# Optimization experiments

Measured on AMD Instinct MI355X. Metric: run time of the kernel, lower is better.

Reference implementation:

```python
import jax, jax.numpy as jnp
import numpy as np
from jax import lax

DIM = 256          # C
D_INNER = 512      # expand * dim
D_STATE = 16       # N
DT_RANK = 32       # ceil(d_inner / 16)
K_CONV = 4


def setup_inputs() -> dict:
    key = jax.random.key(0)
    ks = jax.random.split(key, 20)
    B, C, H, W = 2, DIM, 64, 64
    Di, N, R = D_INNER, D_STATE, DT_RANK
    s = 0.02
    inp = {
        "decoder_feat": jax.random.normal(ks[0], (B, C, H, W), jnp.float32),
        "encoder_feat": jax.random.normal(ks[1], (B, C, H, W), jnp.float32),
        # CrossMambaFusion params
        "dec_w": jax.random.normal(ks[2], (C, 2 * Di), jnp.float32) * s,
        "dec_b": jnp.zeros((2 * Di,), jnp.float32),
        "enc_w": jax.random.normal(ks[3], (C, Di), jnp.float32) * s,
        "enc_b": jnp.zeros((Di,), jnp.float32),
        "out_w": jax.random.normal(ks[4], (Di, C), jnp.float32) * s,
        "out_b": jnp.zeros((C,), jnp.float32),
        "ln_g": jnp.ones((C,), jnp.float32),
        "ln_b": jnp.zeros((C,), jnp.float32),
        # Mamba block params (inner dim = Di, expand=1.0)
        "in_w": jax.random.normal(ks[5], (Di, 2 * Di), jnp.float32) * s,
        "in_b": jnp.zeros((2 * Di,), jnp.float32),
        "conv_w": jax.random.normal(ks[6], (Di, 1, K_CONV), jnp.float32) * 0.1,
        "conv_b": jnp.zeros((Di,), jnp.float32),
        "x_proj_w": jax.random.normal(ks[7], (Di, R + 2 * N), jnp.float32) * s,
        "dt_w": jax.random.normal(ks[8], (R, Di), jnp.float32) * 0.1,
        "dt_b": jax.random.uniform(ks[9], (Di,), jnp.float32, -4.0, -2.0),  # small dt after softplus
        "A_log": jnp.log(jnp.tile(jnp.arange(1, N + 1, dtype=jnp.float32)[None, :], (Di, 1))),
        "D_param": jnp.ones((Di,), jnp.float32),
        "m_out_w": jax.random.normal(ks[10], (Di, Di), jnp.float32) * s,
        "m_out_b": jnp.zeros((Di,), jnp.float32),
    }
    return inp


def _mamba(x, in_w, in_b, conv_w, conv_b, x_proj_w, dt_w, dt_b, A_log, D_param, m_out_w, m_out_b):
    # x: (B, L, Di)
    Bsz, L, Di = x.shape
    N, R = D_STATE, DT_RANK
    xz = x @ in_w + in_b                      # (B, L, 2*Di)
    xm, z = jnp.split(xz, 2, axis=-1)
    # causal depthwise conv over the sequence axis
    xc = jnp.swapaxes(xm, 1, 2)               # (B, Di, L)
    xc = lax.conv_general_dilated(
        xc, conv_w, window_strides=(1,), padding=[(K_CONV - 1, 0)],
        dimension_numbers=("NCH", "OIH", "NCH"), feature_group_count=Di)
    xc = xc + conv_b[None, :, None]
    u = jax.nn.silu(jnp.swapaxes(xc, 1, 2))   # (B, L, Di)
    x_dbl = u @ x_proj_w                      # (B, L, R+2N)
    dt = jax.nn.softplus(x_dbl[..., :R] @ dt_w + dt_b)   # (B, L, Di)
    Bm = x_dbl[..., R:R + N]                  # (B, L, N)
    Cm = x_dbl[..., R + N:]                   # (B, L, N)
    A = -jnp.exp(A_log)                       # (Di, N)

    def step(h, t):
        dt_t, u_t, B_t, C_t = t               # (B,Di),(B,Di),(B,N),(B,N)
        dA = jnp.exp(dt_t[..., None] * A)     # (B, Di, N)
        h = h * dA + (dt_t * u_t)[..., None] * B_t[:, None, :]
        y = jnp.einsum("bdn,bn->bd", h, C_t)
        return h, y

    h0 = jnp.zeros((Bsz, Di, N), x.dtype)
    _, ys = lax.scan(step, h0, (jnp.swapaxes(dt, 0, 1), jnp.swapaxes(u, 0, 1),
                                jnp.swapaxes(Bm, 0, 1), jnp.swapaxes(Cm, 0, 1)))
    y = jnp.swapaxes(ys, 0, 1) + u * D_param  # skip connection via D
    y = y * jax.nn.silu(z)
    return y @ m_out_w + m_out_b


def reference(decoder_feat, encoder_feat, dec_w, dec_b, enc_w, enc_b, out_w, out_b,
              ln_g, ln_b, in_w, in_b, conv_w, conv_b, x_proj_w, dt_w, dt_b,
              A_log, D_param, m_out_w, m_out_b):
    B, C, H, W = decoder_feat.shape
    Di = D_INNER
    dec = jnp.transpose(decoder_feat, (0, 2, 3, 1)).reshape(B, H * W, C)
    enc = jnp.transpose(encoder_feat, (0, 2, 3, 1)).reshape(B, H * W, C)
    dec_proj = dec @ dec_w + dec_b
    dec_x, dec_gate = dec_proj[..., :Di], dec_proj[..., Di:]
    enc_p = enc @ enc_w + enc_b
    combined = dec_x * jax.nn.sigmoid(enc_p) + enc_p          # (B, L, Di)
    processed = _mamba(combined, in_w, in_b, conv_w, conv_b, x_proj_w,
                       dt_w, dt_b, A_log, D_param, m_out_w, m_out_b)
    out = (processed * jax.nn.sigmoid(dec_gate)) @ out_w + out_b
    res = out + dec
    mu = jnp.mean(res, axis=-1, keepdims=True)
    var = jnp.mean(jnp.square(res - mu), axis=-1, keepdims=True)
    res = (res - mu) * lax.rsqrt(var + 1e-5) * ln_g + ln_b
    return jnp.transpose(res.reshape(B, H, W, C), (0, 3, 1, 2))
```

## Files before the change

kernel.cpp:

```cpp
#include <hip/hip_runtime.h>
#include <hip/hip_bf16.h>

typedef __bf16 bf16x8_t __attribute__((ext_vector_type(8)));
typedef float f32x4_t __attribute__((ext_vector_type(4)));

__device__ __forceinline__ float sigmoidf_(float x) { return 1.0f / (1.0f + __expf(-x)); }
__device__ __forceinline__ float siluf_(float x) { return x * sigmoidf_(x); }
__device__ __forceinline__ float softplusf_(float x) {
    return fmaxf(x, 0.0f) + log1pf(__expf(-fabsf(x)));
}
__device__ __forceinline__ float b2f(ushort u) { return __uint_as_float(((unsigned)u) << 16); }

__global__ __launch_bounds__(256) void k_cast_w(
    const float* __restrict__ dec_w, const float* __restrict__ enc_w,
    const float* __restrict__ in_w, const float* __restrict__ m_out_w,
    const float* __restrict__ out_w, const float* __restrict__ x_proj_w,
    const float* __restrict__ dt_w,
    __hip_bfloat16* __restrict__ dec_wT, __hip_bfloat16* __restrict__ enc_wT,
    __hip_bfloat16* __restrict__ in_wT, __hip_bfloat16* __restrict__ m_out_wT,
    __hip_bfloat16* __restrict__ out_wT, __hip_bfloat16* __restrict__ xpwT,
    __hip_bfloat16* __restrict__ dtwT)
{
    int gid = blockIdx.x * 256 + threadIdx.x;
    const float* src; __hip_bfloat16* dst; int lk, N, idx;
    if (gid < 262144)       { src = dec_w;    dst = dec_wT;   lk = 8; N = 1024; idx = gid; }
    else if (gid < 393216)  { src = enc_w;    dst = enc_wT;   lk = 8; N = 512;  idx = gid - 262144; }
    else if (gid < 917504)  { src = in_w;     dst = in_wT;    lk = 9; N = 1024; idx = gid - 393216; }
    else if (gid < 1179648) { src = m_out_w;  dst = m_out_wT; lk = 9; N = 512;  idx = gid - 917504; }
    else if (gid < 1310720) { src = out_w;    dst = out_wT;   lk = 9; N = 256;  idx = gid - 1179648; }
    else if (gid < 1343488) { src = x_proj_w; dst = xpwT;     lk = 9; N = 64;   idx = gid - 1310720; }
    else                    { src = dt_w;     dst = dtwT;     lk = 5; N = 512;  idx = gid - 1343488; }
    int K = 1 << lk;
    int n = idx >> lk, k = idx & (K - 1);
    dst[idx] = __float2bfloat16(src[(size_t)k * N + n]);
}

__global__ __launch_bounds__(256) void k_tr_in(
    const float* __restrict__ dec, const float* __restrict__ enc,
    __hip_bfloat16* __restrict__ decL, __hip_bfloat16* __restrict__ encL)
{
    __shared__ float tile[64][65];
    const int t = threadIdx.x;
    const int ct = blockIdx.x & 3;
    const int lt = (blockIdx.x >> 2) & 63;
    const int sel = blockIdx.x >> 8;
    const int b = sel & 1, ten = sel >> 1;
    const float* src = ten ? enc : dec;
    __hip_bfloat16* dst = ten ? encL : decL;
    const size_t ibase = (size_t)b * 256 * 4096 + (size_t)(ct * 64) * 4096 + (size_t)lt * 64;
#pragma unroll
    for (int i = 0; i < 16; ++i) {
        int c = i * 4 + (t >> 6), l = t & 63;
        tile[c][l] = src[ibase + (size_t)c * 4096 + l];
    }
    __syncthreads();
    const size_t obase = ((size_t)b * 4096 + (size_t)lt * 64) * 256 + ct * 64;
#pragma unroll
    for (int i = 0; i < 16; ++i) {
        int l = i * 4 + (t >> 6), c = t & 63;
        dst[obase + (size_t)l * 256 + c] = __float2bfloat16(tile[c][l]);
    }
}

template <int EPI, int K>
__global__ __launch_bounds__(256) void bgemm(
    const __hip_bfloat16* __restrict__ A, const __hip_bfloat16* __restrict__ Bt,
    const float* __restrict__ bias, void* __restrict__ out0,
    void* __restrict__ out1, const void* __restrict__ extra)
{
    __shared__ ushort At[128 * 32];
    __shared__ ushort Bl[128 * 32];
    const int tid = threadIdx.x;
    const int wave = tid >> 6, lane = tid & 63;
    const int n0 = blockIdx.x * 128, m0 = blockIdx.y * 128;
    const int wm = (wave >> 1) * 64, wn = (wave & 1) * 64;
    f32x4_t acc[4][4] = {};
    const int fr = lane & 15, fq = (lane >> 4) * 8;

    for (int k0 = 0; k0 < K; k0 += 32) {
#pragma unroll
        for (int q = 0; q < 2; ++q) {
            int idx = q * 256 + tid;
            int row = idx >> 2, ch = (idx & 3) * 8;
            uint4 va = *(const uint4*)&A[(size_t)(m0 + row) * K + k0 + ch];
            uint4 vb = *(const uint4*)&Bt[(size_t)(n0 + row) * K + k0 + ch];
            *(uint4*)&At[row * 32 + ch] = va;
            *(uint4*)&Bl[row * 32 + ch] = vb;
        }
        __syncthreads();
        bf16x8_t af[4], bf[4];
#pragma unroll
        for (int i = 0; i < 4; ++i) {
            af[i] = *(bf16x8_t*)&At[(wm + i * 16 + fr) * 32 + fq];
            bf[i] = *(bf16x8_t*)&Bl[(wn + i * 16 + fr) * 32 + fq];
        }
#pragma unroll
        for (int i = 0; i < 4; ++i)
#pragma unroll
            for (int j = 0; j < 4; ++j)
                acc[i][j] = __builtin_amdgcn_mfma_f32_16x16x32_bf16(af[i], bf[j], acc[i][j], 0, 0, 0);
        __syncthreads();
    }

    const int col = lane & 15, rbase = (lane >> 4) * 4;
#pragma unroll
    for (int i = 0; i < 4; ++i) {
#pragma unroll
        for (int j = 0; j < 4; ++j) {
#pragma unroll
            for (int r = 0; r < 4; ++r) {
                int m = m0 + wm + i * 16 + rbase + r;
                int n = n0 + wn + j * 16 + col;
                float v = acc[i][j][r] + bias[n];
                if (EPI == 0) {
                    ((__hip_bfloat16*)out0)[(size_t)m * 512 + n] = __float2bfloat16(v);
                } else if (EPI == 1) {
                    if (n < 512) {
                        float ep = __bfloat162float(((const __hip_bfloat16*)extra)[(size_t)m * 512 + n]);
                        ((__hip_bfloat16*)out0)[(size_t)m * 512 + n] =
                            __float2bfloat16(fmaf(v, sigmoidf_(ep), ep));
                    } else {
                        ((__hip_bfloat16*)out1)[(size_t)m * 512 + (n - 512)] =
                            __float2bfloat16(sigmoidf_(v));
                    }
                } else if (EPI == 2) {
                    if (n < 512)
                        ((__hip_bfloat16*)out0)[(size_t)m * 512 + n] = __float2bfloat16(v);
                    else
                        ((__hip_bfloat16*)out1)[(size_t)m * 512 + (n - 512)] =
                            __float2bfloat16(siluf_(v));
                } else if (EPI == 3) {
                    float g = __bfloat162float(((const __hip_bfloat16*)extra)[(size_t)m * 512 + n]);
                    ((__hip_bfloat16*)out0)[(size_t)m * 512 + n] = __float2bfloat16(v * g);
                } else {
                    float dv = __bfloat162float(((const __hip_bfloat16*)extra)[(size_t)m * 256 + n]);
                    ((float*)out0)[(size_t)m * 256 + n] = v + dv;
                }
            }
        }
    }
}

#define CROWS 16
__global__ __launch_bounds__(256) void k_conv_proj(
    const __hip_bfloat16* __restrict__ xm, const float* __restrict__ conv_w,
    const float* __restrict__ conv_b, const __hip_bfloat16* __restrict__ xpwT,
    const __hip_bfloat16* __restrict__ dtwT, const float* __restrict__ dt_b,
    __hip_bfloat16* __restrict__ u_out, float* __restrict__ Bm,
    float* __restrict__ Cm, float* __restrict__ dt_out)
{
    __shared__ ushort ut[CROWS][512 + 8];
    __shared__ ushort adt[CROWS][32 + 8];
    const int tid = threadIdx.x;
    const int wave = tid >> 6, lane = tid & 63;
    const int bl0 = blockIdx.x * CROWS;
    const int l0 = bl0 & 4095;
    const int fr = lane & 15, fq = (lane >> 4) * 8;
    const int col = lane & 15, rbase = (lane >> 4) * 4;

    {
        const int d0 = tid * 2;
        float cw0[4], cw1[4];
#pragma unroll
        for (int k = 0; k < 4; ++k) {
            cw0[k] = conv_w[d0 * 4 + k];
            cw1[k] = conv_w[d0 * 4 + 4 + k];
        }
        const float cb0 = conv_b[d0], cb1 = conv_b[d0 + 1];
        float xa[CROWS + 3], xb[CROWS + 3];
        const ushort* xs = (const ushort*)xm;
#pragma unroll
        for (int i = 0; i < CROWS + 3; ++i) {
            if (l0 - 3 + i >= 0) {
                ushort2 v = *(const ushort2*)&xs[(size_t)(bl0 - 3 + i) * 512 + d0];
                xa[i] = b2f(v.x); xb[i] = b2f(v.y);
            } else { xa[i] = 0.f; xb[i] = 0.f; }
        }
#pragma unroll
        for (int r = 0; r < CROWS; ++r) {
            float a = cb0, b = cb1;
#pragma unroll
            for (int k = 0; k < 4; ++k) {
                a = fmaf(cw0[k], xa[r + k], a);
                b = fmaf(cw1[k], xb[r + k], b);
            }
            float ua = siluf_(a), ub = siluf_(b);
            ushort2 up = make_ushort2(
                (ushort)(__bfloat16_as_ushort(__float2bfloat16(ua))),
                (ushort)(__bfloat16_as_ushort(__float2bfloat16(ub))));
            *(ushort2*)&ut[r][d0] = up;
            *(ushort2*)&((ushort*)u_out)[(size_t)(bl0 + r) * 512 + d0] = up;
        }
    }
    __syncthreads();

    {
        f32x4_t acc = {};
        const __hip_bfloat16* bp = xpwT + (size_t)(wave * 16 + fr) * 512;
#pragma unroll
        for (int k0 = 0; k0 < 512; k0 += 32) {
            bf16x8_t af = *(bf16x8_t*)&ut[fr][k0 + fq];
            bf16x8_t bf = *(const bf16x8_t*)&bp[k0 + fq];
            acc = __builtin_amdgcn_mfma_f32_16x16x32_bf16(af, bf, acc, 0, 0, 0);
        }
#pragma unroll
        for (int r = 0; r < 4; ++r) {
            int m = rbase + r;
            int n = wave * 16 + col;
            float v = acc[r];
            if (n < 32)      adt[m][n] = (ushort)__bfloat16_as_ushort(__float2bfloat16(v));
            else if (n < 48) Bm[(size_t)(bl0 + m) * 16 + (n - 32)] = v;
            else             Cm[(size_t)(bl0 + m) * 16 + (n - 48)] = v;
        }
    }
    __syncthreads();

    {
        bf16x8_t af = *(bf16x8_t*)&adt[fr][fq];
#pragma unroll
        for (int t = 0; t < 8; ++t) {
            int nt = wave * 8 + t;
            bf16x8_t bf = *(const bf16x8_t*)&dtwT[(size_t)(nt * 16 + fr) * 32 + fq];
            f32x4_t acc = {};
            acc = __builtin_amdgcn_mfma_f32_16x16x32_bf16(af, bf, acc, 0, 0, 0);
#pragma unroll
            for (int r = 0; r < 4; ++r) {
                int m = rbase + r;
                int n = nt * 16 + col;
                dt_out[(size_t)(bl0 + m) * 512 + n] = softplusf_(acc[r] + dt_b[n]);
            }
        }
    }
}

#define CHUNK 32
#define NCHUNK 128

__global__ __launch_bounds__(512) void k_scan_part(
    const float* __restrict__ dt, const __hip_bfloat16* __restrict__ u,
    const float* __restrict__ Bmp, const float* __restrict__ A_log,
    float* __restrict__ hpart, float* __restrict__ decay)
{
    __shared__ float Bs[CHUNK * 16];
    const int d = threadIdx.x;
    const int chunk = blockIdx.x & (NCHUNK - 1);
    const int b = blockIdx.x >> 7;
    const size_t row0 = (size_t)b * 4096 + (size_t)chunk * CHUNK;

    Bs[d] = Bmp[row0 * 16 + d];
    float Av[16];
#pragma unroll
    for (int n = 0; n < 16; n += 4) {
        float4 al = *(const float4*)&A_log[d * 16 + n];
        Av[n + 0] = -__expf(al.x);
        Av[n + 1] = -__expf(al.y);
        Av[n + 2] = -__expf(al.z);
        Av[n + 3] = -__expf(al.w);
    }
    __syncthreads();

    const float* dtp = dt + row0 * 512 + d;
    const __hip_bfloat16* up = u + row0 * 512 + d;
    float h[16] = {};
    float dtsum = 0.f;
    for (int t = 0; t < CHUNK; ++t) {
        float dtv = dtp[(size_t)t * 512];
        float uv = __bfloat162float(up[(size_t)t * 512]);
        float dtu = dtv * uv;
        dtsum += dtv;
        const float* Bt = &Bs[t * 16];
#pragma unroll
        for (int n = 0; n < 16; ++n)
            h[n] = fmaf(h[n], __expf(dtv * Av[n]), dtu * Bt[n]);
    }
    const size_t idx = (((size_t)b * NCHUNK + chunk) * 512 + d) * 16;
#pragma unroll
    for (int n = 0; n < 16; n += 4)
        *(float4*)&hpart[idx + n] = make_float4(h[n], h[n + 1], h[n + 2], h[n + 3]);
#pragma unroll
    for (int n = 0; n < 16; n += 4)
        *(float4*)&decay[idx + n] = make_float4(
            __expf(Av[n] * dtsum), __expf(Av[n + 1] * dtsum),
            __expf(Av[n + 2] * dtsum), __expf(Av[n + 3] * dtsum));
}

__global__ __launch_bounds__(256) void k_scan_comb(
    const float* __restrict__ hpart, const float* __restrict__ decay,
    float* __restrict__ h_in)
{
    const int gid = blockIdx.x * 256 + threadIdx.x;
    const int n = gid & 15;
    const int d = (gid >> 4) & 511;
    const int b = gid >> 13;
    float h = 0.f;
    for (int c = 0; c < NCHUNK; ++c) {
        const size_t idx = (((size_t)b * NCHUNK + c) * 512 + d) * 16 + n;
        h_in[idx] = h;
        h = fmaf(h, decay[idx], hpart[idx]);
    }
}

__global__ __launch_bounds__(512) void k_scan_fin(
    const float* __restrict__ dt, const __hip_bfloat16* __restrict__ u,
    const float* __restrict__ Bmp, const float* __restrict__ Cmp,
    const float* __restrict__ A_log, const float* __restrict__ Dp,
    const __hip_bfloat16* __restrict__ zs, const float* __restrict__ h_in,
    __hip_bfloat16* __restrict__ yout)
{
    __shared__ float Bs[CHUNK * 16];
    __shared__ float Cs[CHUNK * 16];
    const int d = threadIdx.x;
    const int chunk = blockIdx.x & (NCHUNK - 1);
    const int b = blockIdx.x >> 7;
    const size_t row0 = (size_t)b * 4096 + (size_t)chunk * CHUNK;

    Bs[d] = Bmp[row0 * 16 + d];
    Cs[d] = Cmp[row0 * 16 + d];
    float Av[16];
#pragma unroll
    for (int n = 0; n < 16; n += 4) {
        float4 al = *(const float4*)&A_log[d * 16 + n];
        Av[n + 0] = -__expf(al.x);
        Av[n + 1] = -__expf(al.y);
        Av[n + 2] = -__expf(al.z);
        Av[n + 3] = -__expf(al.w);
    }
    const float Dv = Dp[d];
    float h[16];
    const size_t idx = (((size_t)b * NCHUNK + chunk) * 512 + d) * 16;
#pragma unroll
    for (int n = 0; n < 16; n += 4) {
        float4 hv = *(const float4*)&h_in[idx + n];
        h[n] = hv.x; h[n + 1] = hv.y; h[n + 2] = hv.z; h[n + 3] = hv.w;
    }
    __syncthreads();

    const float* dtp = dt + row0 * 512 + d;
    const __hip_bfloat16* up = u + row0 * 512 + d;
    const __hip_bfloat16* zp = zs + row0 * 512 + d;
    __hip_bfloat16* yp = yout + row0 * 512 + d;
    for (int t = 0; t < CHUNK; ++t) {
        float dtv = dtp[(size_t)t * 512];
        float uv = __bfloat162float(up[(size_t)t * 512]);
        float zv = __bfloat162float(zp[(size_t)t * 512]);
        float dtu = dtv * uv;
        const float* Bt = &Bs[t * 16];
        const float* Ct = &Cs[t * 16];
        float y = 0.f;
#pragma unroll
        for (int n = 0; n < 16; ++n) {
            h[n] = fmaf(h[n], __expf(dtv * Av[n]), dtu * Bt[n]);
            y = fmaf(h[n], Ct[n], y);
        }
        yp[(size_t)t * 512] = __float2bfloat16((y + uv * Dv) * zv);
    }
}

__global__ __launch_bounds__(256) void k_ln_t(
    const float* __restrict__ res, const float* __restrict__ ln_g,
    const float* __restrict__ ln_b, float* __restrict__ outp)
{
    __shared__ float r[64 * 257];
    __shared__ float red[64][8];
    __shared__ float mu_s[64], sc_s[64];
    const int tid = threadIdx.x;
    const int b = blockIdx.x >> 6;
    const int l0 = (blockIdx.x & 63) * 64;
    const size_t base = ((size_t)b * 4096 + l0) * 256;

    for (int e = tid; e < 64 * 256; e += 256) {
        int i = e >> 8;
        int c = e & 255;
        r[i * 257 + c] = res[base + (size_t)i * 256 + c];
    }
    __syncthreads();
    {
        int i = tid >> 2, s = tid & 3;
        float ps = 0.f, pq = 0.f;
        for (int c = s * 64; c < s * 64 + 64; ++c) {
            float v = r[i * 257 + c];
            ps += v;
            pq = fmaf(v, v, pq);
        }
        red[i][s] = ps;
        red[i][4 + s] = pq;
    }
    __syncthreads();
    if (tid < 64) {
        float ps = red[tid][0] + red[tid][1] + red[tid][2] + red[tid][3];
        float pq = red[tid][4] + red[tid][5] + red[tid][6] + red[tid][7];
        float mu = ps * (1.0f / 256.0f);
        float var = pq * (1.0f / 256.0f) - mu * mu;
        mu_s[tid] = mu;
        sc_s[tid] = rsqrtf(var + 1e-5f);
    }
    __syncthreads();
    const int il = tid & 63;
    const int cg = tid >> 6;
    const float mu = mu_s[il], sc = sc_s[il];
    for (int c = cg; c < 256; c += 4) {
        float v = (r[il * 257 + c] - mu) * sc * ln_g[c] + ln_b[c];
        outp[(size_t)b * (256 * 4096) + (size_t)c * 4096 + l0 + il] = v;
    }
}

extern "C" void kernel_launch(void* const* d_in, const int* in_sizes, int n_in,
                              void* d_out, int out_size, void* d_ws, size_t ws_size,
                              hipStream_t stream)
{
    const float* decoder_feat = (const float*)d_in[0];
    const float* encoder_feat = (const float*)d_in[1];
    const float* dec_w = (const float*)d_in[2];
    const float* dec_b = (const float*)d_in[3];
    const float* enc_w = (const float*)d_in[4];
    const float* enc_b = (const float*)d_in[5];
    const float* out_w = (const float*)d_in[6];
    const float* out_b = (const float*)d_in[7];
    const float* ln_g = (const float*)d_in[8];
    const float* ln_bb = (const float*)d_in[9];
    const float* in_w = (const float*)d_in[10];
    const float* in_b = (const float*)d_in[11];
    const float* conv_w = (const float*)d_in[12];
    const float* conv_b = (const float*)d_in[13];
    const float* x_proj_w = (const float*)d_in[14];
    const float* dt_w = (const float*)d_in[15];
    const float* dt_b = (const float*)d_in[16];
    const float* A_log = (const float*)d_in[17];
    const float* D_param = (const float*)d_in[18];
    const float* m_out_w = (const float*)d_in[19];
    const float* m_out_b = (const float*)d_in[20];

    float* outp = (float*)d_out;
    char* ws = (char*)d_ws;
    const size_t MB = 1024ull * 1024;
    __hip_bfloat16* decL     = (__hip_bfloat16*)(ws + 0 * MB);
    __hip_bfloat16* encL     = (__hip_bfloat16*)(ws + 4 * MB);
    __hip_bfloat16* dec_wT   = (__hip_bfloat16*)(ws + 8 * MB);
    __hip_bfloat16* enc_wT   = (__hip_bfloat16*)(ws + 9 * MB);
    __hip_bfloat16* in_wT    = (__hip_bfloat16*)(ws + 10 * MB);
    __hip_bfloat16* m_out_wT = (__hip_bfloat16*)(ws + 11 * MB);
    __hip_bfloat16* out_wT   = (__hip_bfloat16*)(ws + 12 * MB);
    __hip_bfloat16* xpwT     = (__hip_bfloat16*)(ws + 12 * MB + 262144);
    __hip_bfloat16* dtwT     = (__hip_bfloat16*)(ws + 12 * MB + 262144 + 65536);
    __hip_bfloat16* enc_pb   = (__hip_bfloat16*)(ws + 13 * MB);
    __hip_bfloat16* combined = (__hip_bfloat16*)(ws + 29 * MB);
    __hip_bfloat16* gate_sig = (__hip_bfloat16*)(ws + 37 * MB);
    __hip_bfloat16* xm = (__hip_bfloat16*)(ws + 53 * MB);
    __hip_bfloat16* z_silu = (__hip_bfloat16*)(ws + 61 * MB);
    __hip_bfloat16* u_buf = (__hip_bfloat16*)(ws + 69 * MB);
    float* dt_buf = (float*)(ws + 77 * MB);
    float* Bm = (float*)(ws + 93 * MB);
    float* Cm = (float*)(ws + 93 * MB + 524288);
    float* hpart = (float*)(ws + 13 * MB);
    float* decay = hpart + 2097152;
    float* h_in  = (float*)xm;
    __hip_bfloat16* y_buf = combined;
    __hip_bfloat16* gated = xm;
    float* res = dt_buf;

    k_cast_w<<<5312, 256, 0, stream>>>(dec_w, enc_w, in_w, m_out_w, out_w, x_proj_w, dt_w,
                                       dec_wT, enc_wT, in_wT, m_out_wT, out_wT, xpwT, dtwT);
    k_tr_in<<<1024, 256, 0, stream>>>(decoder_feat, encoder_feat, decL, encL);
    bgemm<0, 256><<<dim3(4, 64), 256, 0, stream>>>(
        encL, enc_wT, enc_b, enc_pb, nullptr, nullptr);
    bgemm<1, 256><<<dim3(8, 64), 256, 0, stream>>>(
        decL, dec_wT, dec_b, combined, gate_sig, enc_pb);
    bgemm<2, 512><<<dim3(8, 64), 256, 0, stream>>>(
        combined, in_wT, in_b, xm, z_silu, nullptr);
    k_conv_proj<<<512, 256, 0, stream>>>(
        xm, conv_w, conv_b, xpwT, dtwT, dt_b, u_buf, Bm, Cm, dt_buf);
    k_scan_part<<<2 * NCHUNK, 512, 0, stream>>>(dt_buf, u_buf, Bm, A_log, hpart, decay);
    k_scan_comb<<<64, 256, 0, stream>>>(hpart, decay, h_in);
    k_scan_fin<<<2 * NCHUNK, 512, 0, stream>>>(
        dt_buf, u_buf, Bm, Cm, A_log, D_param, z_silu, h_in, y_buf);
    bgemm<3, 512><<<dim3(4, 64), 256, 0, stream>>>(
        y_buf, m_out_wT, m_out_b, gated, nullptr, gate_sig);
    bgemm<4, 512><<<dim3(2, 64), 256, 0, stream>>>(
        gated, out_wT, out_b, res, nullptr, decL);
    k_ln_t<<<128, 256, 0, stream>>>(res, ln_g, ln_bb, outp);
}
```

Measured before the change: 297.1 us.

## Fuse prep kernels, dec/enc projections, and output GEMM with LayerNorm

Merges the weight-cast and input-transpose kernels into one launch. It computes the encoder and decoder projections in a single dual-accumulator GEMM, so enc_p never goes through memory. It also fuses the final output GEMM with the residual add and LayerNorm, so the fp32 residual buffer is no longer written and read back. This saves launches and global traffic, but the fused output kernel runs only 64 blocks of 512 threads with large shared memory, which lowers parallelism on a GPU with many CUs.

```diff
diff --git a/kernel.cpp b/kernel.cpp
--- a/kernel.cpp
+++ b/kernel.cpp
@@ -11,39 +11,39 @@
 }
 __device__ __forceinline__ float b2f(ushort u) { return __uint_as_float(((unsigned)u) << 16); }
 
-__global__ __launch_bounds__(256) void k_cast_w(
+__global__ __launch_bounds__(256) void k_prep(
     const float* __restrict__ dec_w, const float* __restrict__ enc_w,
     const float* __restrict__ in_w, const float* __restrict__ m_out_w,
     const float* __restrict__ out_w, const float* __restrict__ x_proj_w,
     const float* __restrict__ dt_w,
+    const float* __restrict__ dec, const float* __restrict__ enc,
     __hip_bfloat16* __restrict__ dec_wT, __hip_bfloat16* __restrict__ enc_wT,
     __hip_bfloat16* __restrict__ in_wT, __hip_bfloat16* __restrict__ m_out_wT,
     __hip_bfloat16* __restrict__ out_wT, __hip_bfloat16* __restrict__ xpwT,
-    __hip_bfloat16* __restrict__ dtwT)
-{
-    int gid = blockIdx.x * 256 + threadIdx.x;
-    const float* src; __hip_bfloat16* dst; int lk, N, idx;
-    if (gid < 262144)       { src = dec_w;    dst = dec_wT;   lk = 8; N = 1024; idx = gid; }
-    else if (gid < 393216)  { src = enc_w;    dst = enc_wT;   lk = 8; N = 512;  idx = gid - 262144; }
-    else if (gid < 917504)  { src = in_w;     dst = in_wT;    lk = 9; N = 1024; idx = gid - 393216; }
-    else if (gid < 1179648) { src = m_out_w;  dst = m_out_wT; lk = 9; N = 512;  idx = gid - 917504; }
-    else if (gid < 1310720) { src = out_w;    dst = out_wT;   lk = 9; N = 256;  idx = gid - 1179648; }
-    else if (gid < 1343488) { src = x_proj_w; dst = xpwT;     lk = 9; N = 64;   idx = gid - 1310720; }
-    else                    { src = dt_w;     dst = dtwT;     lk = 5; N = 512;  idx = gid - 1343488; }
-    int K = 1 << lk;
-    int n = idx >> lk, k = idx & (K - 1);
-    dst[idx] = __float2bfloat16(src[(size_t)k * N + n]);
-}
-
-__global__ __launch_bounds__(256) void k_tr_in(
-    const float* __restrict__ dec, const float* __restrict__ enc,
+    __hip_bfloat16* __restrict__ dtwT,
     __hip_bfloat16* __restrict__ decL, __hip_bfloat16* __restrict__ encL)
 {
     __shared__ float tile[64][65];
+    if (blockIdx.x < 5312) {
+        int gid = blockIdx.x * 256 + threadIdx.x;
+        const float* src; __hip_bfloat16* dst; int lk, N, idx;
+        if (gid < 262144)       { src = dec_w;    dst = dec_wT;   lk = 8; N = 1024; idx = gid; }
+        else if (gid < 393216)  { src = enc_w;    dst = enc_wT;   lk = 8; N = 512;  idx = gid - 262144; }
+        else if (gid < 917504)  { src = in_w;     dst = in_wT;    lk = 9; N = 1024; idx = gid - 393216; }
+        else if (gid < 1179648) { src = m_out_w;  dst = m_out_wT; lk = 9; N = 512;  idx = gid - 917504; }
+        else if (gid < 1310720) { src = out_w;    dst = out_wT;   lk = 9; N = 256;  idx = gid - 1179648; }
+        else if (gid < 1343488) { src = x_proj_w; dst = xpwT;     lk = 9; N = 64;   idx = gid - 1310720; }
+        else                    { src = dt_w;     dst = dtwT;     lk = 5; N = 512;  idx = gid - 1343488; }
+        int K = 1 << lk;
+        int n = idx >> lk, k = idx & (K - 1);
+        dst[idx] = __float2bfloat16(src[(size_t)k * N + n]);
+        return;
+    }
+    const int bid = blockIdx.x - 5312;
     const int t = threadIdx.x;
-    const int ct = blockIdx.x & 3;
-    const int lt = (blockIdx.x >> 2) & 63;
-    const int sel = blockIdx.x >> 8;
+    const int ct = bid & 3;
+    const int lt = (bid >> 2) & 63;
+    const int sel = bid >> 8;
     const int b = sel & 1, ten = sel >> 1;
     const float* src = ten ? enc : dec;
     __hip_bfloat16* dst = ten ? encL : decL;
@@ -59,6 +59,82 @@
     for (int i = 0; i < 16; ++i) {
         int l = i * 4 + (t >> 6), c = t & 63;
         dst[obase + (size_t)l * 256 + c] = __float2bfloat16(tile[c][l]);
+    }
+}
+
+__global__ __launch_bounds__(256) void k_fuse_in(
+    const __hip_bfloat16* __restrict__ decL, const __hip_bfloat16* __restrict__ encL,
+    const __hip_bfloat16* __restrict__ dec_wT, const __hip_bfloat16* __restrict__ enc_wT,
+    const float* __restrict__ dec_b, const float* __restrict__ enc_b,
+    __hip_bfloat16* __restrict__ combined, __hip_bfloat16* __restrict__ gate_sig)
+{
+    __shared__ ushort Ad[128 * 32], Bd[128 * 32], Ae[128 * 32], Be[128 * 32];
+    const int tid = threadIdx.x;
+    const int wave = tid >> 6, lane = tid & 63;
+    const int n0 = blockIdx.x * 128, m0 = blockIdx.y * 128;
+    const bool dual = (n0 < 512);
+    const int wm = (wave >> 1) * 64, wn = (wave & 1) * 64;
+    f32x4_t accd[4][4] = {}, acce[4][4] = {};
+    const int fr = lane & 15, fq = (lane >> 4) * 8;
+
+    for (int k0 = 0; k0 < 256; k0 += 32) {
+#pragma unroll
+        for (int q = 0; q < 2; ++q) {
+            int idx = q * 256 + tid;
+            int row = idx >> 2, ch = (idx & 3) * 8;
+            *(uint4*)&Ad[row * 32 + ch] = *(const uint4*)&decL[(size_t)(m0 + row) * 256 + k0 + ch];
+            *(uint4*)&Bd[row * 32 + ch] = *(const uint4*)&dec_wT[(size_t)(n0 + row) * 256 + k0 + ch];
+            if (dual) {
+                *(uint4*)&Ae[row * 32 + ch] = *(const uint4*)&encL[(size_t)(m0 + row) * 256 + k0 + ch];
+                *(uint4*)&Be[row * 32 + ch] = *(const uint4*)&enc_wT[(size_t)(n0 + row) * 256 + k0 + ch];
+            }
+        }
+        __syncthreads();
+        bf16x8_t ad[4], bd[4];
+#pragma unroll
+        for (int i = 0; i < 4; ++i) {
+            ad[i] = *(bf16x8_t*)&Ad[(wm + i * 16 + fr) * 32 + fq];
+            bd[i] = *(bf16x8_t*)&Bd[(wn + i * 16 + fr) * 32 + fq];
+        }
+#pragma unroll
+        for (int i = 0; i < 4; ++i)
+#pragma unroll
+            for (int j = 0; j < 4; ++j)
+                accd[i][j] = __builtin_amdgcn_mfma_f32_16x16x32_bf16(ad[i], bd[j], accd[i][j], 0, 0, 0);
+        if (dual) {
+            bf16x8_t ae[4], be[4];
+#pragma unroll
+            for (int i = 0; i < 4; ++i) {
+                ae[i] = *(bf16x8_t*)&Ae[(wm + i * 16 + fr) * 32 + fq];
+                be[i] = *(bf16x8_t*)&Be[(wn + i * 16 + fr) * 32 + fq];
+            }
+#pragma unroll
+            for (int i = 0; i < 4; ++i)
+#pragma unroll
+                for (int j = 0; j < 4; ++j)
+                    acce[i][j] = __builtin_amdgcn_mfma_f32_16x16x32_bf16(ae[i], be[j], acce[i][j], 0, 0, 0);
+        }
+        __syncthreads();
+    }
+
+    const int col = lane & 15, rbase = (lane >> 4) * 4;
+#pragma unroll
+    for (int i = 0; i < 4; ++i) {
+#pragma unroll
+        for (int j = 0; j < 4; ++j) {
+#pragma unroll
+            for (int r = 0; r < 4; ++r) {
+                int m = m0 + wm + i * 16 + rbase + r;
+                int n = n0 + wn + j * 16 + col;
+                float vd = accd[i][j][r] + dec_b[n];
+                if (dual) {
+                    float ve = acce[i][j][r] + enc_b[n];
+                    combined[(size_t)m * 512 + n] = __float2bfloat16(fmaf(vd, sigmoidf_(ve), ve));
+                } else {
+                    gate_sig[(size_t)m * 512 + (n - 512)] = __float2bfloat16(sigmoidf_(vd));
+                }
+            }
+        }
     }
 }
 
@@ -112,29 +188,15 @@
                 int m = m0 + wm + i * 16 + rbase + r;
                 int n = n0 + wn + j * 16 + col;
                 float v = acc[i][j][r] + bias[n];
-                if (EPI == 0) {
-                    ((__hip_bfloat16*)out0)[(size_t)m * 512 + n] = __float2bfloat16(v);
-                } else if (EPI == 1) {
-                    if (n < 512) {
-                        float ep = __bfloat162float(((const __hip_bfloat16*)extra)[(size_t)m * 512 + n]);
-                        ((__hip_bfloat16*)out0)[(size_t)m * 512 + n] =
-                            __float2bfloat16(fmaf(v, sigmoidf_(ep), ep));
-                    } else {
-                        ((__hip_bfloat16*)out1)[(size_t)m * 512 + (n - 512)] =
-                            __float2bfloat16(sigmoidf_(v));
-                    }
-                } else if (EPI == 2) {
+                if (EPI == 2) {
                     if (n < 512)
                         ((__hip_bfloat16*)out0)[(size_t)m * 512 + n] = __float2bfloat16(v);
                     else
                         ((__hip_bfloat16*)out1)[(size_t)m * 512 + (n - 512)] =
                             __float2bfloat16(siluf_(v));
-                } else if (EPI == 3) {
+                } else {
                     float g = __bfloat162float(((const __hip_bfloat16*)extra)[(size_t)m * 512 + n]);
                     ((__hip_bfloat16*)out0)[(size_t)m * 512 + n] = __float2bfloat16(v * g);
-                } else {
-                    float dv = __bfloat162float(((const __hip_bfloat16*)extra)[(size_t)m * 256 + n]);
-                    ((float*)out0)[(size_t)m * 256 + n] = v + dv;
                 }
             }
         }
@@ -356,51 +418,107 @@
     }
 }
 
-__global__ __launch_bounds__(256) void k_ln_t(
-    const float* __restrict__ res, const float* __restrict__ ln_g,
-    const float* __restrict__ ln_b, float* __restrict__ outp)
-{
-    __shared__ float r[64 * 257];
-    __shared__ float red[64][8];
-    __shared__ float mu_s[64], sc_s[64];
+__global__ __launch_bounds__(512) void k_out_ln(
+    const __hip_bfloat16* __restrict__ A, const __hip_bfloat16* __restrict__ Bt,
+    const float* __restrict__ bias, const __hip_bfloat16* __restrict__ decL,
+    const float* __restrict__ ln_g, const float* __restrict__ ln_b,
+    float* __restrict__ outp)
+{
+    __shared__ __align__(16) char sm[70912];
+    ushort* At = (ushort*)sm;
+    ushort* Bl = (ushort*)(sm + 8192);
+    float (*lr)[257] = (float(*)[257])sm;
+    float* lred = (float*)(sm + 65792);
+    float* lmu  = (float*)(sm + 69888);
+    float* lsc  = (float*)(sm + 70144);
+
     const int tid = threadIdx.x;
-    const int b = blockIdx.x >> 6;
-    const int l0 = (blockIdx.x & 63) * 64;
-    const size_t base = ((size_t)b * 4096 + l0) * 256;
-
-    for (int e = tid; e < 64 * 256; e += 256) {
-        int i = e >> 8;
-        int c = e & 255;
-        r[i * 257 + c] = res[base + (size_t)i * 256 + c];
-    }
-    __syncthreads();
-    {
-        int i = tid >> 2, s = tid & 3;
-        float ps = 0.f, pq = 0.f;
-        for (int c = s * 64; c < s * 64 + 64; ++c) {
-            float v = r[i * 257 + c];
-            ps += v;
-            pq = fmaf(v, v, pq);
-        }
-        red[i][s] = ps;
-        red[i][4 + s] = pq;
-    }
-    __syncthreads();
-    if (tid < 64) {
-        float ps = red[tid][0] + red[tid][1] + red[tid][2] + red[tid][3];
-        float pq = red[tid][4] + red[tid][5] + red[tid][6] + red[tid][7];
-        float mu = ps * (1.0f / 256.0f);
-        float var = pq * (1.0f / 256.0f) - mu * mu;
-        mu_s[tid] = mu;
-        sc_s[tid] = rsqrtf(var + 1e-5f);
-    }
-    __syncthreads();
-    const int il = tid & 63;
-    const int cg = tid >> 6;
-    const float mu = mu_s[il], sc = sc_s[il];
-    for (int c = cg; c < 256; c += 4) {
-        float v = (r[il * 257 + c] - mu) * sc * ln_g[c] + ln_b[c];
-        outp[(size_t)b * (256 * 4096) + (size_t)c * 4096 + l0 + il] = v;
+    const int wave = tid >> 6, lane = tid & 63;
+    const int m0 = blockIdx.x * 128;
+    const int wm = (wave >> 2) * 64, wn = (wave & 3) * 64;
+    f32x4_t acc[4][4] = {};
+    const int fr = lane & 15, fq = (lane >> 4) * 8;
+
+    for (int k0 = 0; k0 < 512; k0 += 32) {
+        {
+            int row = tid >> 2, ch = (tid & 3) * 8;
+            *(uint4*)&At[row * 32 + ch] = *(const uint4*)&A[(size_t)(m0 + row) * 512 + k0 + ch];
+        }
+#pragma unroll
+        for (int q = 0; q < 2; ++q) {
+            int idx = q * 512 + tid;
+            int row = idx >> 2, ch = (idx & 3) * 8;
+            *(uint4*)&Bl[row * 32 + ch] = *(const uint4*)&Bt[(size_t)row * 512 + k0 + ch];
+        }
+        __syncthreads();
+        bf16x8_t af[4], bf[4];
+#pragma unroll
+        for (int i = 0; i < 4; ++i) {
+            af[i] = *(bf16x8_t*)&At[(wm + i * 16 + fr) * 32 + fq];
+            bf[i] = *(bf16x8_t*)&Bl[(wn + i * 16 + fr) * 32 + fq];
+        }
+#pragma unroll
+        for (int i = 0; i < 4; ++i)
+#pragma unroll
+            for (int j = 0; j < 4; ++j)
+                acc[i][j] = __builtin_amdgcn_mfma_f32_16x16x32_bf16(af[i], bf[j], acc[i][j], 0, 0, 0);
+        __syncthreads();
+    }
+
+    const int col = lane & 15, rbase = (lane >> 4) * 4;
+    for (int mh = 0; mh < 2; ++mh) {
+        if ((wm >> 6) == mh) {
+#pragma unroll
+            for (int i = 0; i < 4; ++i)
+#pragma unroll
+                for (int j = 0; j < 4; ++j)
+#pragma unroll
+                    for (int r = 0; r < 4; ++r) {
+                        int rl = i * 16 + rbase + r;
+                        int n = wn + j * 16 + col;
+                        int m = m0 + mh * 64 + rl;
+                        float dv = b2f(((const ushort*)decL)[(size_t)m * 256 + n]);
+                        lr[rl][n] = acc[i][j][r] + bias[n] + dv;
+                    }
+        }
+        __syncthreads();
+        {
+            int i = tid >> 3, s = tid & 7;
+            float ps = 0.f, pq = 0.f;
+#pragma unroll 8
+            for (int k = 0; k < 32; ++k) {
+                float v = lr[i][s + 8 * k];
+                ps += v;
+                pq = fmaf(v, v, pq);
+            }
+            lred[i * 16 + s] = ps;
+            lred[i * 16 + 8 + s] = pq;
+        }
+        __syncthreads();
+        if (tid < 64) {
+            float ps = 0.f, pq = 0.f;
+#pragma unroll
+            for (int s = 0; s < 8; ++s) {
+                ps += lred[tid * 16 + s];
+                pq += lred[tid * 16 + 8 + s];
+            }
+            float mu = ps * (1.0f / 256.0f);
+            float var = pq * (1.0f / 256.0f) - mu * mu;
+            lmu[tid] = mu;
+            lsc[tid] = rsqrtf(var + 1e-5f);
+        }
+        __syncthreads();
+        {
+            int l = tid & 63;
+            int m = m0 + mh * 64 + l;
+            int bb = m >> 12, lpos = m & 4095;
+            float mu = lmu[l], sc = lsc[l];
+            for (int c = tid >> 6; c < 256; c += 8) {
+                float v = (lr[l][c] - mu) * sc * ln_g[c] + ln_b[c];
+                outp[(size_t)bb * (256 * 4096) + (size_t)c * 4096 + lpos] = v;
+            }
+        }
+        __syncthreads();
     }
 }
 
@@ -442,29 +560,26 @@
     __hip_bfloat16* out_wT   = (__hip_bfloat16*)(ws + 12 * MB);
     __hip_bfloat16* xpwT     = (__hip_bfloat16*)(ws + 12 * MB + 262144);
     __hip_bfloat16* dtwT     = (__hip_bfloat16*)(ws + 12 * MB + 262144 + 65536);
-    __hip_bfloat16* enc_pb   = (__hip_bfloat16*)(ws + 13 * MB);
+    float* hpart             = (float*)(ws + 13 * MB);
+    float* decay             = hpart + 2097152;
     __hip_bfloat16* combined = (__hip_bfloat16*)(ws + 29 * MB);
     __hip_bfloat16* gate_sig = (__hip_bfloat16*)(ws + 37 * MB);
-    __hip_bfloat16* xm = (__hip_bfloat16*)(ws + 53 * MB);
-    __hip_bfloat16* z_silu = (__hip_bfloat16*)(ws + 61 * MB);
-    __hip_bfloat16* u_buf = (__hip_bfloat16*)(ws + 69 * MB);
-    float* dt_buf = (float*)(ws + 77 * MB);
-    float* Bm = (float*)(ws + 93 * MB);
-    float* Cm = (float*)(ws + 93 * MB + 524288);
-    float* hpart = (float*)(ws + 13 * MB);
-    float* decay = hpart + 2097152;
-    float* h_in  = (float*)xm;
-    __hip_bfloat16* y_buf = combined;
-    __hip_bfloat16* gated = xm;
-    float* res = dt_buf;
-
-    k_cast_w<<<5312, 256, 0, stream>>>(dec_w, enc_w, in_w, m_out_w, out_w, x_proj_w, dt_w,
-                                       dec_wT, enc_wT, in_wT, m_out_wT, out_wT, xpwT, dtwT);
-    k_tr_in<<<1024, 256, 0, stream>>>(decoder_feat, encoder_feat, decL, encL);
-    bgemm<0, 256><<<dim3(4, 64), 256, 0, stream>>>(
-        encL, enc_wT, enc_b, enc_pb, nullptr, nullptr);
-    bgemm<1, 256><<<dim3(8, 64), 256, 0, stream>>>(
-        decL, dec_wT, dec_b, combined, gate_sig, enc_pb);
+    __hip_bfloat16* xm       = (__hip_bfloat16*)(ws + 53 * MB);
+    __hip_bfloat16* z_silu   = (__hip_bfloat16*)(ws + 61 * MB);
+    __hip_bfloat16* u_buf    = (__hip_bfloat16*)(ws + 69 * MB);
+    float* dt_buf            = (float*)(ws + 77 * MB);
+    float* Bm                = (float*)(ws + 93 * MB);
+    float* Cm                = (float*)(ws + 93 * MB + 524288);
+    float* h_in              = (float*)xm;
+    __hip_bfloat16* y_buf    = combined;
+    __hip_bfloat16* gated    = xm;
+
+    k_prep<<<6336, 256, 0, stream>>>(
+        dec_w, enc_w, in_w, m_out_w, out_w, x_proj_w, dt_w,
+        decoder_feat, encoder_feat,
+        dec_wT, enc_wT, in_wT, m_out_wT, out_wT, xpwT, dtwT, decL, encL);
+    k_fuse_in<<<dim3(8, 64), 256, 0, stream>>>(
+        decL, encL, dec_wT, enc_wT, dec_b, enc_b, combined, gate_sig);
     bgemm<2, 512><<<dim3(8, 64), 256, 0, stream>>>(
         combined, in_wT, in_b, xm, z_silu, nullptr);
     k_conv_proj<<<512, 256, 0, stream>>>(
@@ -475,7 +590,6 @@
         dt_buf, u_buf, Bm, Cm, A_log, D_param, z_silu, h_in, y_buf);
     bgemm<3, 512><<<dim3(4, 64), 256, 0, stream>>>(
         y_buf, m_out_wT, m_out_b, gated, nullptr, gate_sig);
-    bgemm<4, 512><<<dim3(2, 64), 256, 0, stream>>>(
-        gated, out_wT, out_b, res, nullptr, decL);
-    k_ln_t<<<128, 256, 0, stream>>>(res, ln_g, ln_bb, outp);
-}
+    k_out_ln<<<64, 512, 0, stream>>>(
+        gated, out_wT, out_b, decL, ln_g, ln_bb, outp);
+}
```

Result: slower. 316.5 us (+6.5%).

## Fuse out-proj GEMM with LayerNorm, merge prep kernels, store chunk dt sums

Applied to the files above, without the earlier changes.

Replaces the final output GEMM plus separate LayerNorm/transpose kernel with one kernel that computes the 256-wide row GEMM per 64-row tile, adds the residual and bias, and normalises in registers before writing transposed output. This removes the fp32 round trip of the residual buffer. The weight-cast and input-transpose kernels are merged into a single launch. The scan stores one dt sum per chunk instead of 16 decay values, and the combine step recomputes the exps. The fused kernel runs only 128 blocks and writes the transposed output with a strided pattern, which may underuse the GPU.

```diff
diff --git a/kernel.cpp b/kernel.cpp
--- a/kernel.cpp
+++ b/kernel.cpp
@@ -11,39 +11,39 @@
 }
 __device__ __forceinline__ float b2f(ushort u) { return __uint_as_float(((unsigned)u) << 16); }
 
-__global__ __launch_bounds__(256) void k_cast_w(
+__global__ __launch_bounds__(256) void k_prep(
     const float* __restrict__ dec_w, const float* __restrict__ enc_w,
     const float* __restrict__ in_w, const float* __restrict__ m_out_w,
     const float* __restrict__ out_w, const float* __restrict__ x_proj_w,
     const float* __restrict__ dt_w,
+    const float* __restrict__ dec, const float* __restrict__ enc,
     __hip_bfloat16* __restrict__ dec_wT, __hip_bfloat16* __restrict__ enc_wT,
     __hip_bfloat16* __restrict__ in_wT, __hip_bfloat16* __restrict__ m_out_wT,
     __hip_bfloat16* __restrict__ out_wT, __hip_bfloat16* __restrict__ xpwT,
-    __hip_bfloat16* __restrict__ dtwT)
-{
-    int gid = blockIdx.x * 256 + threadIdx.x;
-    const float* src; __hip_bfloat16* dst; int lk, N, idx;
-    if (gid < 262144)       { src = dec_w;    dst = dec_wT;   lk = 8; N = 1024; idx = gid; }
-    else if (gid < 393216)  { src = enc_w;    dst = enc_wT;   lk = 8; N = 512;  idx = gid - 262144; }
-    else if (gid < 917504)  { src = in_w;     dst = in_wT;    lk = 9; N = 1024; idx = gid - 393216; }
-    else if (gid < 1179648) { src = m_out_w;  dst = m_out_wT; lk = 9; N = 512;  idx = gid - 917504; }
-    else if (gid < 1310720) { src = out_w;    dst = out_wT;   lk = 9; N = 256;  idx = gid - 1179648; }
-    else if (gid < 1343488) { src = x_proj_w; dst = xpwT;     lk = 9; N = 64;   idx = gid - 1310720; }
-    else                    { src = dt_w;     dst = dtwT;     lk = 5; N = 512;  idx = gid - 1343488; }
-    int K = 1 << lk;
-    int n = idx >> lk, k = idx & (K - 1);
-    dst[idx] = __float2bfloat16(src[(size_t)k * N + n]);
-}
-
-__global__ __launch_bounds__(256) void k_tr_in(
-    const float* __restrict__ dec, const float* __restrict__ enc,
+    __hip_bfloat16* __restrict__ dtwT,
     __hip_bfloat16* __restrict__ decL, __hip_bfloat16* __restrict__ encL)
 {
     __shared__ float tile[64][65];
+    if (blockIdx.x < 5312) {
+        int gid = blockIdx.x * 256 + threadIdx.x;
+        const float* src; __hip_bfloat16* dst; int lk, N, idx;
+        if (gid < 262144)       { src = dec_w;    dst = dec_wT;   lk = 8; N = 1024; idx = gid; }
+        else if (gid < 393216)  { src = enc_w;    dst = enc_wT;   lk = 8; N = 512;  idx = gid - 262144; }
+        else if (gid < 917504)  { src = in_w;     dst = in_wT;    lk = 9; N = 1024; idx = gid - 393216; }
+        else if (gid < 1179648) { src = m_out_w;  dst = m_out_wT; lk = 9; N = 512;  idx = gid - 917504; }
+        else if (gid < 1310720) { src = out_w;    dst = out_wT;   lk = 9; N = 256;  idx = gid - 1179648; }
+        else if (gid < 1343488) { src = x_proj_w; dst = xpwT;     lk = 9; N = 64;   idx = gid - 1310720; }
+        else                    { src = dt_w;     dst = dtwT;     lk = 5; N = 512;  idx = gid - 1343488; }
+        int K = 1 << lk;
+        int n = idx >> lk, k = idx & (K - 1);
+        dst[idx] = __float2bfloat16(src[(size_t)k * N + n]);
+        return;
+    }
+    const int bid = blockIdx.x - 5312;
     const int t = threadIdx.x;
-    const int ct = blockIdx.x & 3;
-    const int lt = (blockIdx.x >> 2) & 63;
-    const int sel = blockIdx.x >> 8;
+    const int ct = bid & 3;
+    const int lt = (bid >> 2) & 63;
+    const int sel = bid >> 8;
     const int b = sel & 1, ten = sel >> 1;
     const float* src = ten ? enc : dec;
     __hip_bfloat16* dst = ten ? encL : decL;
@@ -129,12 +129,9 @@
                     else
                         ((__hip_bfloat16*)out1)[(size_t)m * 512 + (n - 512)] =
                             __float2bfloat16(siluf_(v));
-                } else if (EPI == 3) {
+                } else {
                     float g = __bfloat162float(((const __hip_bfloat16*)extra)[(size_t)m * 512 + n]);
                     ((__hip_bfloat16*)out0)[(size_t)m * 512 + n] = __float2bfloat16(v * g);
-                } else {
-                    float dv = __bfloat162float(((const __hip_bfloat16*)extra)[(size_t)m * 256 + n]);
-                    ((float*)out0)[(size_t)m * 256 + n] = v + dv;
                 }
             }
         }
@@ -239,7 +236,7 @@
 __global__ __launch_bounds__(512) void k_scan_part(
     const float* __restrict__ dt, const __hip_bfloat16* __restrict__ u,
     const float* __restrict__ Bmp, const float* __restrict__ A_log,
-    float* __restrict__ hpart, float* __restrict__ decay)
+    float* __restrict__ hpart, float* __restrict__ dtsums)
 {
     __shared__ float Bs[CHUNK * 16];
     const int d = threadIdx.x;
@@ -273,30 +270,29 @@
         for (int n = 0; n < 16; ++n)
             h[n] = fmaf(h[n], __expf(dtv * Av[n]), dtu * Bt[n]);
     }
-    const size_t idx = (((size_t)b * NCHUNK + chunk) * 512 + d) * 16;
+    const size_t sidx = ((size_t)b * NCHUNK + chunk) * 512 + d;
+    const size_t idx = sidx * 16;
 #pragma unroll
     for (int n = 0; n < 16; n += 4)
         *(float4*)&hpart[idx + n] = make_float4(h[n], h[n + 1], h[n + 2], h[n + 3]);
-#pragma unroll
-    for (int n = 0; n < 16; n += 4)
-        *(float4*)&decay[idx + n] = make_float4(
-            __expf(Av[n] * dtsum), __expf(Av[n + 1] * dtsum),
-            __expf(Av[n + 2] * dtsum), __expf(Av[n + 3] * dtsum));
+    dtsums[sidx] = dtsum;
 }
 
 __global__ __launch_bounds__(256) void k_scan_comb(
-    const float* __restrict__ hpart, const float* __restrict__ decay,
-    float* __restrict__ h_in)
+    const float* __restrict__ hpart, const float* __restrict__ dtsums,
+    const float* __restrict__ A_log, float* __restrict__ h_in)
 {
     const int gid = blockIdx.x * 256 + threadIdx.x;
     const int n = gid & 15;
     const int d = (gid >> 4) & 511;
     const int b = gid >> 13;
+    const float Av = -__expf(A_log[d * 16 + n]);
     float h = 0.f;
     for (int c = 0; c < NCHUNK; ++c) {
-        const size_t idx = (((size_t)b * NCHUNK + c) * 512 + d) * 16 + n;
+        const size_t sidx = ((size_t)b * NCHUNK + c) * 512 + d;
+        const size_t idx = sidx * 16 + n;
         h_in[idx] = h;
-        h = fmaf(h, decay[idx], hpart[idx]);
+        h = fmaf(h, __expf(Av * dtsums[sidx]), hpart[idx]);
     }
 }
 
@@ -356,51 +352,98 @@
     }
 }
 
-__global__ __launch_bounds__(256) void k_ln_t(
-    const float* __restrict__ res, const float* __restrict__ ln_g,
-    const float* __restrict__ ln_b, float* __restrict__ outp)
-{
-    __shared__ float r[64 * 257];
-    __shared__ float red[64][8];
-    __shared__ float mu_s[64], sc_s[64];
+__global__ __launch_bounds__(256) void k_out_ln(
+    const __hip_bfloat16* __restrict__ A, const __hip_bfloat16* __restrict__ Bt,
+    const float* __restrict__ bias, const __hip_bfloat16* __restrict__ decL,
+    const float* __restrict__ ln_g, const float* __restrict__ ln_b,
+    float* __restrict__ outp)
+{
+    __shared__ ushort At[64 * 32];
+    __shared__ ushort Bl[256 * 32];
+    __shared__ float red[4][64][2];
+    __shared__ float lmu[64], lsc[64];
     const int tid = threadIdx.x;
-    const int b = blockIdx.x >> 6;
-    const int l0 = (blockIdx.x & 63) * 64;
-    const size_t base = ((size_t)b * 4096 + l0) * 256;
-
-    for (int e = tid; e < 64 * 256; e += 256) {
-        int i = e >> 8;
-        int c = e & 255;
-        r[i * 257 + c] = res[base + (size_t)i * 256 + c];
-    }
-    __syncthreads();
-    {
-        int i = tid >> 2, s = tid & 3;
-        float ps = 0.f, pq = 0.f;
-        for (int c = s * 64; c < s * 64 + 64; ++c) {
-            float v = r[i * 257 + c];
-            ps += v;
-            pq = fmaf(v, v, pq);
-        }
-        red[i][s] = ps;
-        red[i][4 + s] = pq;
+    const int wave = tid >> 6, lane = tid & 63;
+    const int m0 = blockIdx.x * 64;
+    const int wn = wave * 64;
+    f32x4_t acc[4][4] = {};
+    const int fr = lane & 15, fq = (lane >> 4) * 8;
+
+    for (int k0 = 0; k0 < 512; k0 += 32) {
+        {
+            int row = tid >> 2, ch = (tid & 3) * 8;
+            *(uint4*)&At[row * 32 + ch] = *(const uint4*)&A[(size_t)(m0 + row) * 512 + k0 + ch];
+        }
+#pragma unroll
+        for (int q = 0; q < 4; ++q) {
+            int idx = q * 256 + tid;
+            int row = idx >> 2, ch = (idx & 3) * 8;
+            *(uint4*)&Bl[row * 32 + ch] = *(const uint4*)&Bt[(size_t)row * 512 + k0 + ch];
+        }
+        __syncthreads();
+        bf16x8_t af[4], bf[4];
+#pragma unroll
+        for (int i = 0; i < 4; ++i) {
+            af[i] = *(bf16x8_t*)&At[(i * 16 + fr) * 32 + fq];
+            bf[i] = *(bf16x8_t*)&Bl[(wn + i * 16 + fr) * 32 + fq];
+        }
+#pragma unroll
+        for (int i = 0; i < 4; ++i)
+#pragma unroll
+            for (int j = 0; j < 4; ++j)
+                acc[i][j] = __builtin_amdgcn_mfma_f32_16x16x32_bf16(af[i], bf[j], acc[i][j], 0, 0, 0);
+        __syncthreads();
+    }
+
+    const int col = lane & 15, rbase = (lane >> 4) * 4;
+#pragma unroll
+    for (int i = 0; i < 4; ++i) {
+#pragma unroll
+        for (int r = 0; r < 4; ++r) {
+            int ml = i * 16 + rbase + r;
+            int m = m0 + ml;
+            float s = 0.f, sq = 0.f;
+#pragma unroll
+            for (int j = 0; j < 4; ++j) {
+                int n = wn + j * 16 + col;
+                float dv = b2f(((const ushort*)decL)[(size_t)m * 256 + n]);
+                float v = acc[i][j][r] + bias[n] + dv;
+                acc[i][j][r] = v;
+                s += v;
+                sq = fmaf(v, v, sq);
+            }
+            s += __shfl_xor(s, 1);  sq += __shfl_xor(sq, 1);
+            s += __shfl_xor(s, 2);  sq += __shfl_xor(sq, 2);
+            s += __shfl_xor(s, 4);  sq += __shfl_xor(sq, 4);
+            s += __shfl_xor(s, 8);  sq += __shfl_xor(sq, 8);
+            if (col == 0) { red[wave][ml][0] = s; red[wave][ml][1] = sq; }
+        }
     }
     __syncthreads();
     if (tid < 64) {
-        float ps = red[tid][0] + red[tid][1] + red[tid][2] + red[tid][3];
-        float pq = red[tid][4] + red[tid][5] + red[tid][6] + red[tid][7];
-        float mu = ps * (1.0f / 256.0f);
-        float var = pq * (1.0f / 256.0f) - mu * mu;
-        mu_s[tid] = mu;
-        sc_s[tid] = rsqrtf(var + 1e-5f);
-    }
-    __syncthreads();
-    const int il = tid & 63;
-    const int cg = tid >> 6;
-    const float mu = mu_s[il], sc = sc_s[il];
-    for (int c = cg; c < 256; c += 4) {
-        float v = (r[il * 257 + c] - mu) * sc * ln_g[c] + ln_b[c];
-        outp[(size_t)b * (256 * 4096) + (size_t)c * 4096 + l0 + il] = v;
+        float s  = red[0][tid][0] + red[1][tid][0] + red[2][tid][0] + red[3][tid][0];
+        float sq = red[0][tid][1] + red[1][tid][1] + red[2][tid][1] + red[3][tid][1];
+        float mu = s * (1.0f / 256.0f);
+        float var = sq * (1.0f / 256.0f) - mu * mu;
+        lmu[tid] = mu;
+        lsc[tid] = rsqrtf(var + 1e-5f);
+    }
+    __syncthreads();
+    const int bb = m0 >> 12;
+    const int lpos0 = m0 & 4095;
+#pragma unroll
+    for (int i = 0; i < 4; ++i) {
+#pragma unroll
+        for (int r = 0; r < 4; ++r) {
+            int ml = i * 16 + rbase + r;
+            float mu = lmu[ml], sc = lsc[ml];
+#pragma unroll
+            for (int j = 0; j < 4; ++j) {
+                int n = wn + j * 16 + col;
+                float v = (acc[i][j][r] - mu) * sc * ln_g[n] + ln_b[n];
+                outp[(size_t)bb * (256 * 4096) + (size_t)n * 4096 + lpos0 + ml] = v;
+            }
+        }
     }
 }
 
@@ -445,22 +488,22 @@
     __hip_bfloat16* enc_pb   = (__hip_bfloat16*)(ws + 13 * MB);
     __hip_bfloat16* combined = (__hip_bfloat16*)(ws + 29 * MB);
     __hip_bfloat16* gate_sig = (__hip_bfloat16*)(ws + 37 * MB);
-    __hip_bfloat16* xm = (__hip_bfloat16*)(ws + 53 * MB);
-    __hip_bfloat16* z_silu = (__hip_bfloat16*)(ws + 61 * MB);
-    __hip_bfloat16* u_buf = (__hip_bfloat16*)(ws + 69 * MB);
-    float* dt_buf = (float*)(ws + 77 * MB);
-    float* Bm = (float*)(ws + 93 * MB);
-    float* Cm = (float*)(ws + 93 * MB + 524288);
-    float* hpart = (float*)(ws + 13 * MB);
-    float* decay = hpart + 2097152;
-    float* h_in  = (float*)xm;
+    __hip_bfloat16* xm       = (__hip_bfloat16*)(ws + 53 * MB);
+    __hip_bfloat16* z_silu   = (__hip_bfloat16*)(ws + 61 * MB);
+    __hip_bfloat16* u_buf    = (__hip_bfloat16*)(ws + 69 * MB);
+    float* dt_buf            = (float*)(ws + 77 * MB);
+    float* Bm                = (float*)(ws + 93 * MB);
+    float* Cm                = (float*)(ws + 93 * MB + 524288);
+    float* hpart  = (float*)(ws + 13 * MB);
+    float* dtsums = (float*)(ws + 21 * MB);
+    float* h_in   = (float*)xm;
     __hip_bfloat16* y_buf = combined;
     __hip_bfloat16* gated = xm;
-    float* res = dt_buf;
-
-    k_cast_w<<<5312, 256, 0, stream>>>(dec_w, enc_w, in_w, m_out_w, out_w, x_proj_w, dt_w,
-                                       dec_wT, enc_wT, in_wT, m_out_wT, out_wT, xpwT, dtwT);
-    k_tr_in<<<1024, 256, 0, stream>>>(decoder_feat, encoder_feat, decL, encL);
+
+    k_prep<<<6336, 256, 0, stream>>>(
+        dec_w, enc_w, in_w, m_out_w, out_w, x_proj_w, dt_w,
+        decoder_feat, encoder_feat,
+        dec_wT, enc_wT, in_wT, m_out_wT, out_wT, xpwT, dtwT, decL, encL);
     bgemm<0, 256><<<dim3(4, 64), 256, 0, stream>>>(
         encL, enc_wT, enc_b, enc_pb, nullptr, nullptr);
     bgemm<1, 256><<<dim3(8, 64), 256, 0, stream>>>(
@@ -469,13 +512,12 @@
         combined, in_wT, in_b, xm, z_silu, nullptr);
     k_conv_proj<<<512, 256, 0, stream>>>(
         xm, conv_w, conv_b, xpwT, dtwT, dt_b, u_buf, Bm, Cm, dt_buf);
-    k_scan_part<<<2 * NCHUNK, 512, 0, stream>>>(dt_buf, u_buf, Bm, A_log, hpart, decay);
-    k_scan_comb<<<64, 256, 0, stream>>>(hpart, decay, h_in);
+    k_scan_part<<<2 * NCHUNK, 512, 0, stream>>>(dt_buf, u_buf, Bm, A_log, hpart, dtsums);
+    k_scan_comb<<<64, 256, 0, stream>>>(hpart, dtsums, A_log, h_in);
     k_scan_fin<<<2 * NCHUNK, 512, 0, stream>>>(
         dt_buf, u_buf, Bm, Cm, A_log, D_param, z_silu, h_in, y_buf);
     bgemm<3, 512><<<dim3(4, 64), 256, 0, stream>>>(
         y_buf, m_out_wT, m_out_b, gated, nullptr, gate_sig);
-    bgemm<4, 512><<<dim3(2, 64), 256, 0, stream>>>(
-        gated, out_wT, out_b, res, nullptr, decL);
-    k_ln_t<<<128, 256, 0, stream>>>(res, ln_g, ln_bb, outp);
-}
+    k_out_ln<<<128, 256, 0, stream>>>(
+        gated, out_wT, out_b, decL, ln_g, ln_bb, outp);
+}
```

New measurement: 289.2 us. 2.7% less time.
